# Kernel optimization log

Hardware: AMD Instinct MI355X
Metric: run time of the kernel (lower is better)

## Reference

```python
import jax, jax.numpy as jnp
import numpy as np

T = 5          # Newton iterations (init kwarg T)
EPS = 1e-05    # covariance regularizer (init kwarg eps)


def setup_inputs() -> dict:
    key = jax.random.key(0)
    k1, k2 = jax.random.split(key)
    B, C, H, W = 64, 128, 56, 56
    x = jax.random.normal(k1, (B, C, H, W), dtype=jnp.float32)
    running_rot = jax.random.normal(k2, (C, C), dtype=jnp.float32)
    return {"x": x, "running_rot": running_rot}


def reference(x, running_rot):
    # Concept Whitening forward (training-mode batch statistics), channels_first.
    # 1) IterNorm ZCA whitening via T Newton iterations on the CxC covariance.
    # 2) Rotation by the (non-trainable) running rotation matrix.
    B, C, H, W = x.shape
    m = B * H * W
    # (C, m): channels as rows, all samples/locations as columns
    xt = x.transpose(1, 0, 2, 3).reshape(C, m)
    mean = jnp.mean(xt, axis=1, keepdims=True)
    xc = xt - mean
    I = jnp.eye(C, dtype=x.dtype)
    Sigma = EPS * I + (xc @ xc.T) / m            # (C, C)
    rTr = 1.0 / jnp.trace(Sigma)                 # trace normalization
    SigmaN = Sigma * rTr
    P = I
    for _ in range(T):                           # Newton iteration for Sigma^{-1/2}
        P = 0.5 * (3.0 * P - P @ P @ P @ SigmaN)
    wm = P * jnp.sqrt(rTr)                       # whitening matrix Sigma^{-1/2}
    xn = wm @ xc                                 # whitened activations (C, m)
    x_hat = xn.reshape(C, B, H, W).transpose(1, 0, 2, 3)  # (B, C, H, W)
    # rotate into concept-aligned basis: out[b,d,h,w] = sum_c rot[d,c] * x_hat[b,c,h,w]
    out = jnp.einsum('bchw,dc->bdhw', x_hat, running_rot)
    return out
```

## Files before the change

### kernel.cpp

```cpp
#include <hip/hip_runtime.h>
#include <math.h>

#define HW 3136
#define NCH224 896
#define M_TOT 200704.0f
#define EPSV 1e-5f

typedef __attribute__((ext_vector_type(8))) short bf16x8;
typedef __attribute__((ext_vector_type(4))) short short4v;
typedef __attribute__((ext_vector_type(4))) float f32x4;

__device__ inline unsigned short f2bf(float f) {
  unsigned u = __float_as_uint(f);
  u += 0x7FFFu + ((u >> 16) & 1u);
  return (unsigned short)(u >> 16);
}

__global__ __launch_bounds__(512, 4) void gram_k(const float* __restrict__ x,
                                                 float* __restrict__ partG,
                                                 float* __restrict__ partS,
                                                 int slots) {
  __shared__ unsigned short xs[128 * 232];
  const int t = threadIdx.x;
  const int lm = t & 15, quad = (t >> 4) & 3, w = t >> 6;
  const int row0 = w * 16;

  f32x4 acc[8];
  f32x4 sacc;
  const f32x4 z = {0.f, 0.f, 0.f, 0.f};
  sacc = z;
#pragma unroll
  for (int j = 0; j < 8; ++j) acc[j] = z;
  bf16x8 ones;
#pragma unroll
  for (int j = 0; j < 8; ++j) ones[j] = (short)0x3F80;

  for (int chunk = blockIdx.x; chunk < NCH224; chunk += slots) {
    const int b = chunk / 14;
    const int s0 = (chunk % 14) * 224;
    const float* base = x + (size_t)(b * 128) * HW + s0;

    float4 buf[14];
#pragma unroll
    for (int i = 0; i < 14; ++i) {
      const int id = t + i * 512;
      const int c = id / 56;
      const int qi = id - c * 56;
      buf[i] = *(const float4*)(base + (size_t)c * HW + 4 * qi);
    }
#pragma unroll
    for (int i = 0; i < 14; ++i) {
      const int id = t + i * 512;
      const int c = id / 56;
      const int qi = id - c * 56;
      uint2 dw;
      dw.x = (unsigned)f2bf(buf[i].x) | ((unsigned)f2bf(buf[i].y) << 16);
      dw.y = (unsigned)f2bf(buf[i].z) | ((unsigned)f2bf(buf[i].w) << 16);
      *(uint2*)&xs[c * 232 + 4 * qi] = dw;
    }
    __syncthreads();

#pragma unroll
    for (int ks = 0; ks < 7; ++ks) {
      const int ko = ks * 32 + quad * 8;
      const bf16x8 a0 = *(const bf16x8*)&xs[(row0 + lm) * 232 + ko];
      sacc = __builtin_amdgcn_mfma_f32_16x16x32_bf16(a0, ones, sacc, 0, 0, 0);
#pragma unroll
      for (int tj = 0; tj < 8; ++tj) {
        const bf16x8 bf = *(const bf16x8*)&xs[(tj * 16 + lm) * 232 + ko];
        acc[tj] = __builtin_amdgcn_mfma_f32_16x16x32_bf16(a0, bf, acc[tj], 0, 0, 0);
      }
    }
    __syncthreads();
  }

  float* pg = partG + (size_t)blockIdx.x * 16384;
#pragma unroll
  for (int tj = 0; tj < 8; ++tj)
#pragma unroll
    for (int r = 0; r < 4; ++r)
      pg[(row0 + quad * 4 + r) * 128 + tj * 16 + lm] = acc[tj][r];
  if (lm == 0) {
#pragma unroll
    for (int r = 0; r < 4; ++r)
      partS[blockIdx.x * 128 + row0 + quad * 4 + r] = sacc[r];
  }
}

__global__ __launch_bounds__(256) void reduce1_k(const float* __restrict__ partG,
                                                 const float* __restrict__ partS,
                                                 float* __restrict__ part2,
                                                 float* __restrict__ part2S,
                                                 int slots) {
  const int t = threadIdx.x;
  const int sg = blockIdx.x & 31;
  const int eg = blockIdx.x >> 5;
  const int e4 = eg * 1024 + t * 4;
  float ax = 0.f, ay = 0.f, az = 0.f, aw = 0.f;
#pragma unroll 4
  for (int s = sg; s < slots; s += 32) {
    const float4 v = *(const float4*)(partG + (size_t)s * 16384 + e4);
    ax += v.x; ay += v.y; az += v.z; aw += v.w;
  }
  *(float4*)(part2 + (size_t)sg * 16384 + e4) = make_float4(ax, ay, az, aw);
  if (eg == 0 && t < 128) {
    float sa = 0.f;
    for (int s = sg; s < slots; s += 32) sa += partS[s * 128 + t];
    part2S[sg * 128 + t] = sa;
  }
}

__global__ __launch_bounds__(256) void sigred_k(const float* __restrict__ part2,
                                                const float* __restrict__ part2S,
                                                float* __restrict__ Sigma,
                                                float* __restrict__ traceP,
                                                float* __restrict__ meanOut) {
  __shared__ float SbL[128];
  __shared__ float red[256];
  const int t = threadIdx.x;
  if (t < 128) {
    float sa = 0.f;
#pragma unroll
    for (int sg = 0; sg < 32; ++sg) sa += part2S[sg * 128 + t];
    SbL[t] = sa;
    if (blockIdx.x == 0) meanOut[t] = sa * (1.0f / M_TOT);
  }
  __syncthreads();
  const int e4 = blockIdx.x * 1024 + t * 4;
  float ax = 0.f, ay = 0.f, az = 0.f, aw = 0.f;
#pragma unroll
  for (int sg = 0; sg < 32; ++sg) {
    const float4 v = *(const float4*)(part2 + (size_t)sg * 16384 + e4);
    ax += v.x; ay += v.y; az += v.z; aw += v.w;
  }
  const int r = e4 >> 7, c0 = e4 & 127;
  const float rm = 1.0f / M_TOT;
  const float sr = SbL[r] * rm;
  float s4[4];
  s4[0] = (ax - sr * SbL[c0 + 0]) * rm;
  s4[1] = (ay - sr * SbL[c0 + 1]) * rm;
  s4[2] = (az - sr * SbL[c0 + 2]) * rm;
  s4[3] = (aw - sr * SbL[c0 + 3]) * rm;
  float trl = 0.f;
#pragma unroll
  for (int j = 0; j < 4; ++j) {
    if (c0 + j == r) { s4[j] += EPSV; trl = s4[j]; }
  }
  *(float4*)(Sigma + e4) = make_float4(s4[0], s4[1], s4[2], s4[3]);
  red[t] = trl;
  __syncthreads();
  for (int off = 128; off > 0; off >>= 1) {
    if (t < off) red[t] += red[t + off];
    __syncthreads();
  }
  if (t == 0) traceP[blockIdx.x] = red[0];
}

__global__ __launch_bounds__(256) void newton1_k(const float* __restrict__ Sig,
                                                 const float* __restrict__ traceP,
                                                 float* __restrict__ Pout) {
  __shared__ float s1[8 * 132];
  __shared__ float s2[8 * 132];
  __shared__ float red[256 * 17];
  const int t = threadIdx.x;
  const int ct = t & 31;
  const int rt = (t >> 5) & 1;
  const int kt = t >> 6;
  const int rg0 = blockIdx.x * 8;
  const int ra = rg0 + 4 * rt;
  float tr = 0.f;
#pragma unroll
  for (int i = 0; i < 16; ++i) tr += traceP[i];
  const float rTr = 1.0f / tr;
  const float nh = -0.5f * rTr;
  float a[4][4];

#pragma unroll
  for (int i = 0; i < 4; ++i)
#pragma unroll
    for (int j = 0; j < 4; ++j) a[i][j] = 0.f;
#pragma unroll 4
  for (int k = kt * 32; k < kt * 32 + 32; ++k) {
    const float4 sa4 = *(const float4*)(Sig + k * 128 + ra);
    const float4 sb4 = *(const float4*)(Sig + k * 128 + 4 * ct);
    float aA[4] = {nh * sa4.x, nh * sa4.y, nh * sa4.z, nh * sa4.w};
    float bA[4] = {nh * sb4.x, nh * sb4.y, nh * sb4.z, nh * sb4.w};
#pragma unroll
    for (int i = 0; i < 4; ++i) if (ra + i == k) aA[i] += 1.5f;
#pragma unroll
    for (int j = 0; j < 4; ++j) if (4 * ct + j == k) bA[j] += 1.5f;
#pragma unroll
    for (int i = 0; i < 4; ++i)
#pragma unroll
      for (int j = 0; j < 4; ++j) a[i][j] += aA[i] * bA[j];
  }
#pragma unroll
  for (int i = 0; i < 4; ++i)
#pragma unroll
    for (int j = 0; j < 4; ++j) red[t * 17 + i * 4 + j] = a[i][j];
  __syncthreads();
  if (t < 64) {
#pragma unroll
    for (int u = 1; u < 4; ++u)
#pragma unroll
      for (int i = 0; i < 4; ++i)
#pragma unroll
        for (int j = 0; j < 4; ++j)
          a[i][j] += red[(t + 64 * u) * 17 + i * 4 + j];
#pragma unroll
    for (int i = 0; i < 4; ++i)
#pragma unroll
      for (int j = 0; j < 4; ++j)
        s1[(4 * rt + i) * 132 + 4 * ct + j] = a[i][j];
  }
  __syncthreads();

#pragma unroll
  for (int i = 0; i < 4; ++i)
#pragma unroll
    for (int j = 0; j < 4; ++j) a[i][j] = 0.f;
#pragma unroll 4
  for (int k = kt * 32; k < kt * 32 + 32; ++k) {
    float aA[4];
#pragma unroll
    for (int i = 0; i < 4; ++i) aA[i] = s1[(4 * rt + i) * 132 + k];
    const float4 sb4 = *(const float4*)(Sig + k * 128 + 4 * ct);
    float bA[4] = {nh * sb4.x, nh * sb4.y, nh * sb4.z, nh * sb4.w};
#pragma unroll
    for (int j = 0; j < 4; ++j) if (4 * ct + j == k) bA[j] += 1.5f;
#pragma unroll
    for (int i = 0; i < 4; ++i)
#pragma unroll
      for (int j = 0; j < 4; ++j) a[i][j] += aA[i] * bA[j];
  }
  __syncthreads();
#pragma unroll
  for (int i = 0; i < 4; ++i)
#pragma unroll
    for (int j = 0; j < 4; ++j) red[t * 17 + i * 4 + j] = a[i][j];
  __syncthreads();
  if (t < 64) {
#pragma unroll
    for (int u = 1; u < 4; ++u)
#pragma unroll
      for (int i = 0; i < 4; ++i)
#pragma unroll
        for (int j = 0; j < 4; ++j)
          a[i][j] += red[(t + 64 * u) * 17 + i * 4 + j];
#pragma unroll
    for (int i = 0; i < 4; ++i)
#pragma unroll
      for (int j = 0; j < 4; ++j)
        s2[(4 * rt + i) * 132 + 4 * ct + j] = a[i][j];
  }
  __syncthreads();

#pragma unroll
  for (int i = 0; i < 4; ++i)
#pragma unroll
    for (int j = 0; j < 4; ++j) a[i][j] = 0.f;
#pragma unroll 4
  for (int k = kt * 32; k < kt * 32 + 32; ++k) {
    float aA[4];
#pragma unroll
    for (int i = 0; i < 4; ++i) aA[i] = s2[(4 * rt + i) * 132 + k];
    const float4 bv = *(const float4*)(Sig + k * 128 + 4 * ct);
    const float bA[4] = {bv.x, bv.y, bv.z, bv.w};
#pragma unroll
    for (int i = 0; i < 4; ++i)
#pragma unroll
      for (int j = 0; j < 4; ++j) a[i][j] += aA[i] * bA[j];
  }
  __syncthreads();
#pragma unroll
  for (int i = 0; i < 4; ++i)
#pragma unroll
    for (int j = 0; j < 4; ++j) red[t * 17 + i * 4 + j] = a[i][j];
  __syncthreads();
  if (t < 64) {
#pragma unroll
    for (int u = 1; u < 4; ++u)
#pragma unroll
      for (int i = 0; i < 4; ++i)
#pragma unroll
        for (int j = 0; j < 4; ++j)
          a[i][j] += red[(t + 64 * u) * 17 + i * 4 + j];
#pragma unroll
    for (int i = 0; i < 4; ++i) {
      const int rg = rg0 + 4 * rt + i;
      const float4 sv = *(const float4*)(Sig + rg * 128 + 4 * ct);
      float p1v[4] = {nh * sv.x, nh * sv.y, nh * sv.z, nh * sv.w};
#pragma unroll
      for (int j = 0; j < 4; ++j) if (4 * ct + j == rg) p1v[j] += 1.5f;
      *(float4*)(Pout + rg * 128 + 4 * ct) =
          make_float4(0.5f * (3.f * p1v[0] - rTr * a[i][0]),
                      0.5f * (3.f * p1v[1] - rTr * a[i][1]),
                      0.5f * (3.f * p1v[2] - rTr * a[i][2]),
                      0.5f * (3.f * p1v[3] - rTr * a[i][3]));
    }
  }
}

__global__ __launch_bounds__(256) void newton_k(const float* __restrict__ P,
                                                const float* __restrict__ Sig,
                                                const float* __restrict__ traceP,
                                                float* __restrict__ Pout) {
  __shared__ float s1[8 * 132];
  __shared__ float s2[8 * 132];
  __shared__ float red[256 * 17];
  const int t = threadIdx.x;
  const int ct = t & 31;
  const int rt = (t >> 5) & 1;
  const int kt = t >> 6;
  const int rg0 = blockIdx.x * 8;
  float tr = 0.f;
#pragma unroll
  for (int i = 0; i < 16; ++i) tr += traceP[i];
  const float rTr = 1.0f / tr;
  float a[4][4];

#pragma unroll
  for (int i = 0; i < 4; ++i)
#pragma unroll
    for (int j = 0; j < 4; ++j) a[i][j] = 0.f;
#pragma unroll 4
  for (int k = kt * 32; k < kt * 32 + 32; ++k) {
    const float4 av = *(const float4*)(P + k * 128 + rg0 + 4 * rt);
    const float4 bv = *(const float4*)(P + k * 128 + 4 * ct);
    const float aA[4] = {av.x, av.y, av.z, av.w};
    const float bA[4] = {bv.x, bv.y, bv.z, bv.w};
#pragma unroll
    for (int i = 0; i < 4; ++i)
#pragma unroll
      for (int j = 0; j < 4; ++j) a[i][j] += aA[i] * bA[j];
  }
#pragma unroll
  for (int i = 0; i < 4; ++i)
#pragma unroll
    for (int j = 0; j < 4; ++j) red[t * 17 + i * 4 + j] = a[i][j];
  __syncthreads();
  if (t < 64) {
#pragma unroll
    for (int u = 1; u < 4; ++u)
#pragma unroll
      for (int i = 0; i < 4; ++i)
#pragma unroll
        for (int j = 0; j < 4; ++j)
          a[i][j] += red[(t + 64 * u) * 17 + i * 4 + j];
#pragma unroll
    for (int i = 0; i < 4; ++i)
#pragma unroll
      for (int j = 0; j < 4; ++j)
        s1[(4 * rt + i) * 132 + 4 * ct + j] = a[i][j];
  }
  __syncthreads();

#pragma unroll
  for (int i = 0; i < 4; ++i)
#pragma unroll
    for (int j = 0; j < 4; ++j) a[i][j] = 0.f;
#pragma unroll 4
  for (int k = kt * 32; k < kt * 32 + 32; ++k) {
    float aA[4];
#pragma unroll
    for (int i = 0; i < 4; ++i) aA[i] = s1[(4 * rt + i) * 132 + k];
    const float4 bv = *(const float4*)(P + k * 128 + 4 * ct);
    const float bA[4] = {bv.x, bv.y, bv.z, bv.w};
#pragma unroll
    for (int i = 0; i < 4; ++i)
#pragma unroll
      for (int j = 0; j < 4; ++j) a[i][j] += aA[i] * bA[j];
  }
  __syncthreads();
#pragma unroll
  for (int i = 0; i < 4; ++i)
#pragma unroll
    for (int j = 0; j < 4; ++j) red[t * 17 + i * 4 + j] = a[i][j];
  __syncthreads();
  if (t < 64) {
#pragma unroll
    for (int u = 1; u < 4; ++u)
#pragma unroll
      for (int i = 0; i < 4; ++i)
#pragma unroll
        for (int j = 0; j < 4; ++j)
          a[i][j] += red[(t + 64 * u) * 17 + i * 4 + j];
#pragma unroll
    for (int i = 0; i < 4; ++i)
#pragma unroll
      for (int j = 0; j < 4; ++j)
        s2[(4 * rt + i) * 132 + 4 * ct + j] = a[i][j];
  }
  __syncthreads();

#pragma unroll
  for (int i = 0; i < 4; ++i)
#pragma unroll
    for (int j = 0; j < 4; ++j) a[i][j] = 0.f;
#pragma unroll 4
  for (int k = kt * 32; k < kt * 32 + 32; ++k) {
    float aA[4];
#pragma unroll
    for (int i = 0; i < 4; ++i) aA[i] = s2[(4 * rt + i) * 132 + k];
    const float4 bv = *(const float4*)(Sig + k * 128 + 4 * ct);
    const float bA[4] = {bv.x, bv.y, bv.z, bv.w};
#pragma unroll
    for (int i = 0; i < 4; ++i)
#pragma unroll
      for (int j = 0; j < 4; ++j) a[i][j] += aA[i] * bA[j];
  }
  __syncthreads();
#pragma unroll
  for (int i = 0; i < 4; ++i)
#pragma unroll
    for (int j = 0; j < 4; ++j) red[t * 17 + i * 4 + j] = a[i][j];
  __syncthreads();
  if (t < 64) {
#pragma unroll
    for (int u = 1; u < 4; ++u)
#pragma unroll
      for (int i = 0; i < 4; ++i)
#pragma unroll
        for (int j = 0; j < 4; ++j)
          a[i][j] += red[(t + 64 * u) * 17 + i * 4 + j];
#pragma unroll
    for (int i = 0; i < 4; ++i) {
      const int rg = rg0 + 4 * rt + i;
      const float4 pv = *(const float4*)(P + rg * 128 + 4 * ct);
      *(float4*)(Pout + rg * 128 + 4 * ct) =
          make_float4(0.5f * (3.f * pv.x - rTr * a[i][0]),
                      0.5f * (3.f * pv.y - rTr * a[i][1]),
                      0.5f * (3.f * pv.z - rTr * a[i][2]),
                      0.5f * (3.f * pv.w - rTr * a[i][3]));
    }
  }
}

__global__ __launch_bounds__(256) void rotmt_k(const float* __restrict__ rot,
                                               const float* __restrict__ P,
                                               const float* __restrict__ mean,
                                               const float* __restrict__ traceP,
                                               unsigned short* __restrict__ Mbf,
                                               float* __restrict__ bias) {
  const int t = threadIdx.x;
  const int r = t >> 5;
  const int dg = blockIdx.x * 8 + r;
  const int c0 = (t & 31) * 4;
  const float* rrow = rot + dg * 128;
  float tr = 0.f;
#pragma unroll
  for (int i = 0; i < 16; ++i) tr += traceP[i];
  const float sc = sqrtf(1.0f / tr);

  float ax = 0, ay = 0, az = 0, aw = 0;
#pragma unroll 4
  for (int k = 0; k < 128; ++k) {
    const float a = rrow[k];
    const float4 bv = *(const float4*)(P + k * 128 + c0);
    ax += a * bv.x; ay += a * bv.y; az += a * bv.z; aw += a * bv.w;
  }
  ax *= sc; ay *= sc; az *= sc; aw *= sc;
  uint2 dw;
  dw.x = (unsigned)f2bf(ax) | ((unsigned)f2bf(ay) << 16);
  dw.y = (unsigned)f2bf(az) | ((unsigned)f2bf(aw) << 16);
  *(uint2*)&Mbf[dg * 128 + c0] = dw;
  const float4 mv = *(const float4*)(mean + c0);
  float p = ax * mv.x + ay * mv.y + az * mv.z + aw * mv.w;
  for (int off = 16; off > 0; off >>= 1) p += __shfl_down(p, off, 32);
  if ((t & 31) == 0) bias[dg] = p;
}

#define MSTR 136
#define XSTR 132
__global__ __launch_bounds__(256, 3) void apply_k(const float* __restrict__ x,
                                                  const unsigned short* __restrict__ Mbf,
                                                  const float* __restrict__ bias,
                                                  float* __restrict__ out) {
  __shared__ unsigned short Ms[128 * MSTR];
  __shared__ unsigned short xsB[64 * XSTR];
  const int t = threadIdx.x;
  const int lm = t & 15, quad = (t >> 4) & 3, w = t >> 6;
  const int b = blockIdx.x / 49;
  const int s0 = (blockIdx.x % 49) * 64;

#pragma unroll
  for (int i = 0; i < 8; ++i) {
    const int e = i * 256 + t;
    const int row = e >> 4, oct = e & 15;
    *(uint4*)&Ms[row * MSTR + oct * 8] =
        *(const uint4*)(Mbf + row * 128 + oct * 8);
  }
#pragma unroll
  for (int i = 0; i < 4; ++i) {
    const int p = 16 * i + (t >> 4);
    const int q = t & 15;
    const float* px = x + (size_t)(b * 128 + 2 * p) * HW + s0 + 4 * q;
    const float4 fa = *(const float4*)px;
    const float4 fb = *(const float4*)(px + HW);
    const float faA[4] = {fa.x, fa.y, fa.z, fa.w};
    const float fbA[4] = {fb.x, fb.y, fb.z, fb.w};
#pragma unroll
    for (int r = 0; r < 4; ++r) {
      const unsigned dw =
          (unsigned)f2bf(faA[r]) | ((unsigned)f2bf(fbA[r]) << 16);
      *(unsigned*)&xsB[(4 * q + r) * XSTR + 2 * p] = dw;
    }
  }
  float biasr[2][4];
#pragma unroll
  for (int i = 0; i < 2; ++i)
#pragma unroll
    for (int r = 0; r < 4; ++r)
      biasr[i][r] = bias[(2 * w + i) * 16 + quad * 4 + r];
  __syncthreads();

  const f32x4 z = {0.f, 0.f, 0.f, 0.f};
  f32x4 acc[2][4];
#pragma unroll
  for (int i = 0; i < 2; ++i)
#pragma unroll
    for (int sj = 0; sj < 4; ++sj) acc[i][sj] = z;

#pragma unroll
  for (int ks = 0; ks < 4; ++ks) {
    const int ko = ks * 32 + quad * 8;
    const bf16x8 a0 = *(const bf16x8*)&Ms[((2 * w + 0) * 16 + lm) * MSTR + ko];
    const bf16x8 a1 = *(const bf16x8*)&Ms[((2 * w + 1) * 16 + lm) * MSTR + ko];
#pragma unroll
    for (int sj = 0; sj < 4; ++sj) {
      const short4v blo = *(const short4v*)&xsB[(sj * 16 + lm) * XSTR + ko];
      const short4v bhi = *(const short4v*)&xsB[(sj * 16 + lm) * XSTR + ko + 4];
      const bf16x8 bf = __builtin_shufflevector(blo, bhi, 0, 1, 2, 3, 4, 5, 6, 7);
      acc[0][sj] = __builtin_amdgcn_mfma_f32_16x16x32_bf16(a0, bf, acc[0][sj], 0, 0, 0);
      acc[1][sj] = __builtin_amdgcn_mfma_f32_16x16x32_bf16(a1, bf, acc[1][sj], 0, 0, 0);
    }
  }
#pragma unroll
  for (int i = 0; i < 2; ++i)
#pragma unroll
    for (int r = 0; r < 4; ++r) {
      const int d = (2 * w + i) * 16 + quad * 4 + r;
      float* orow = out + (size_t)(b * 128 + d) * HW + s0 + lm;
#pragma unroll
      for (int sj = 0; sj < 4; ++sj)
        orow[sj * 16] = acc[i][sj][r] - biasr[i][r];
    }
}

extern "C" void kernel_launch(void* const* d_in, const int* in_sizes, int n_in,
                              void* d_out, int out_size, void* d_ws,
                              size_t ws_size, hipStream_t stream) {
  const float* x = (const float*)d_in[0];
  const float* rot = (const float*)d_in[1];
  float* out = (float*)d_out;
  float* ws = (float*)d_ws;

  float* Sigma  = ws;
  float* Pa     = ws + 16384;
  float* Pb     = ws + 32768;
  unsigned short* Mbf = (unsigned short*)(ws + 49152);
  float* Sb     = ws + 57344;
  float* bias   = ws + 57472;
  float* traceP = ws + 57600;
  float* part2  = ws + 57616;
  float* part2S = ws + 57616 + 524288;
  float* partG  = ws + 57616 + 524288 + 4096;

  const size_t wsf = ws_size / 4;
  long avail = (long)wsf - (57616 + 524288 + 4096);
  int slots = (int)(avail / (16384 + 128));
  if (slots > NCH224) slots = NCH224;
  if (slots < 1) slots = 1;
  float* partS = partG + (size_t)slots * 16384;

  gram_k<<<slots, 512, 0, stream>>>(x, partG, partS, slots);
  reduce1_k<<<512, 256, 0, stream>>>(partG, partS, part2, part2S, slots);
  sigred_k<<<16, 256, 0, stream>>>(part2, part2S, Sigma, traceP, Sb);
  newton1_k<<<16, 256, 0, stream>>>(Sigma, traceP, Pb);
  newton_k<<<16, 256, 0, stream>>>(Pb, Sigma, traceP, Pa);
  newton_k<<<16, 256, 0, stream>>>(Pa, Sigma, traceP, Pb);
  newton_k<<<16, 256, 0, stream>>>(Pb, Sigma, traceP, Pa);
  rotmt_k<<<16, 256, 0, stream>>>(rot, Pa, Sb, traceP, Mbf, bias);
  apply_k<<<3136, 256, 0, stream>>>(x, Mbf, bias, out);
}
```

Measured before the change: 297.3 us.

## Exploit Gram symmetry: store/reduce only upper-triangular tiles, halve partial slots

The Gram partial kernel now writes only the upper-triangular 16x16 tiles of each block's 128x128 partial, and the first reduction kernel processes only those 36 tiles, remapping thread groups to triangular tile indices. The final Sigma reduction reads lower-triangular tiles transposed from the upper half. The slot cap also drops from 896 to 448, so each Gram block covers more chunks and there is half as much partial data to write and reduce. The aim is to cut memory traffic in the partial-sum reduction, at the cost of strided, uncoalesced reads for the lower-triangle entries and fewer, longer Gram blocks.

```diff
diff --git a/kernel.cpp b/kernel.cpp
--- a/kernel.cpp
+++ b/kernel.cpp
@@ -76,10 +76,13 @@
 
   float* pg = partG + (size_t)blockIdx.x * 16384;
 #pragma unroll
-  for (int tj = 0; tj < 8; ++tj)
-#pragma unroll
-    for (int r = 0; r < 4; ++r)
-      pg[(row0 + quad * 4 + r) * 128 + tj * 16 + lm] = acc[tj][r];
+  for (int tj = 0; tj < 8; ++tj) {
+    if (tj >= w) {
+#pragma unroll
+      for (int r = 0; r < 4; ++r)
+        pg[(row0 + quad * 4 + r) * 128 + tj * 16 + lm] = acc[tj][r];
+    }
+  }
   if (lm == 0) {
 #pragma unroll
     for (int r = 0; r < 4; ++r)
@@ -94,16 +97,23 @@
                                                  int slots) {
   const int t = threadIdx.x;
   const int sg = blockIdx.x & 31;
-  const int eg = blockIdx.x >> 5;
-  const int e4 = eg * 1024 + t * 4;
+  const int tg = blockIdx.x >> 5;
+  const int ti = tg * 4 + (t >> 6);
+  int tr = 0, rem = ti;
+  while (rem >= 8 - tr) { rem -= 8 - tr; ++tr; }
+  const int tc = tr + rem;
+  const int f = t & 63;
+  const int rr = f >> 2, c4 = f & 3;
+  const int off = (tr * 16 + rr) * 128 + tc * 16 + c4 * 4;
+
   float ax = 0.f, ay = 0.f, az = 0.f, aw = 0.f;
 #pragma unroll 4
   for (int s = sg; s < slots; s += 32) {
-    const float4 v = *(const float4*)(partG + (size_t)s * 16384 + e4);
+    const float4 v = *(const float4*)(partG + (size_t)s * 16384 + off);
     ax += v.x; ay += v.y; az += v.z; aw += v.w;
   }
-  *(float4*)(part2 + (size_t)sg * 16384 + e4) = make_float4(ax, ay, az, aw);
-  if (eg == 0 && t < 128) {
+  *(float4*)(part2 + (size_t)sg * 16384 + off) = make_float4(ax, ay, az, aw);
+  if (tg == 0 && t < 128) {
     float sa = 0.f;
     for (int s = sg; s < slots; s += 32) sa += partS[s * 128 + t];
     part2S[sg * 128 + t] = sa;
@@ -127,13 +137,25 @@
   }
   __syncthreads();
   const int e4 = blockIdx.x * 1024 + t * 4;
+  const int r = e4 >> 7, c0 = e4 & 127;
+  const int tr = r >> 4, tc = c0 >> 4;
   float ax = 0.f, ay = 0.f, az = 0.f, aw = 0.f;
-#pragma unroll
-  for (int sg = 0; sg < 32; ++sg) {
-    const float4 v = *(const float4*)(part2 + (size_t)sg * 16384 + e4);
-    ax += v.x; ay += v.y; az += v.z; aw += v.w;
-  }
-  const int r = e4 >> 7, c0 = e4 & 127;
+  if (tc >= tr) {
+#pragma unroll
+    for (int sg = 0; sg < 32; ++sg) {
+      const float4 v = *(const float4*)(part2 + (size_t)sg * 16384 + e4);
+      ax += v.x; ay += v.y; az += v.z; aw += v.w;
+    }
+  } else {
+#pragma unroll
+    for (int sg = 0; sg < 32; ++sg) {
+      const float* p = part2 + (size_t)sg * 16384 + r;
+      ax += p[(c0 + 0) * 128];
+      ay += p[(c0 + 1) * 128];
+      az += p[(c0 + 2) * 128];
+      aw += p[(c0 + 3) * 128];
+    }
+  }
   const float rm = 1.0f / M_TOT;
   const float sr = SbL[r] * rm;
   float s4[4];
@@ -569,12 +591,12 @@
   const size_t wsf = ws_size / 4;
   long avail = (long)wsf - (57616 + 524288 + 4096);
   int slots = (int)(avail / (16384 + 128));
-  if (slots > NCH224) slots = NCH224;
+  if (slots > 448) slots = 448;
   if (slots < 1) slots = 1;
   float* partS = partG + (size_t)slots * 16384;
 
   gram_k<<<slots, 512, 0, stream>>>(x, partG, partS, slots);
-  reduce1_k<<<512, 256, 0, stream>>>(partG, partS, part2, part2S, slots);
+  reduce1_k<<<288, 256, 0, stream>>>(partG, partS, part2, part2S, slots);
   sigred_k<<<16, 256, 0, stream>>>(part2, part2S, Sigma, traceP, Sb);
   newton1_k<<<16, 256, 0, stream>>>(Sigma, traceP, Pb);
   newton_k<<<16, 256, 0, stream>>>(Pb, Sigma, traceP, Pa);
```

New measurement: 298.7 us. No clear change (+0.4%).
